# Kernel optimization log

Measured on AMD Instinct MI355X. Metric: run time of the kernel, lower is better.

## Reference

```python
import jax, jax.numpy as jnp
import numpy as np

B = 16
D = 512
LENGTHS = [2048 + 256 * i for i in range(B)]  # sum = 63488 tokens (incl. cls per bag)


def _index_maps(lengths):
    # Static (numpy) index maps for ragged <-> padded layout. Each bag's row 0 is a
    # cls token (left untouched); rows 1..L-1 are the conv body.
    lengths = [int(l) for l in np.asarray(lengths).tolist()]
    offs = np.cumsum([0] + lengths)
    lens_b = [l - 1 for l in lengths]            # body lengths after removing cls
    Lmax = max(lens_b)
    Bn = len(lengths)
    pad_src = np.zeros((Bn, Lmax), dtype=np.int32)   # flat x row gathered into [b,t]
    pad_mask = np.zeros((Bn, Lmax), dtype=np.float32)
    body_pos_list, body_b_list, body_t_list = [], [], []
    for i, L in enumerate(lens_b):
        rows = np.arange(offs[i] + 1, offs[i] + 1 + L)
        pad_src[i, :L] = rows
        pad_mask[i, :L] = 1.0
        body_pos_list.append(rows)
        body_b_list.append(np.full(L, i, dtype=np.int32))
        body_t_list.append(np.arange(L, dtype=np.int32))
    body_pos = np.concatenate(body_pos_list)   # flat positions of body tokens
    body_b = np.concatenate(body_b_list)
    body_t = np.concatenate(body_t_list)
    return pad_src, pad_mask, body_pos, body_b, body_t


def _dwconv(xp, w, b):
    # Depthwise 'same' conv1d. xp: [B, D, Lmax], w: [D, 1, k] (torch layout), b: [D].
    y = jax.lax.conv_general_dilated(
        xp, w, window_strides=(1,), padding='SAME',
        feature_group_count=xp.shape[1],
        dimension_numbers=('NCH', 'OIH', 'NCH'))
    return y + b[None, :, None]


def setup_inputs():
    key = jax.random.key(0)
    ks = jax.random.split(key, 7)
    total = sum(LENGTHS)
    x = jax.random.normal(ks[0], (total, D), jnp.float32)
    def u(k, shape, fan):  # torch Conv1d default init: U(-1/sqrt(fan_in*k), ...)
        bound = 1.0 / np.sqrt(fan)
        return jax.random.uniform(k, shape, jnp.float32, -bound, bound)
    w3, b3 = u(ks[1], (D, 1, 3), 3), u(ks[2], (D,), 3)
    w5, b5 = u(ks[3], (D, 1, 5), 5), u(ks[4], (D,), 5)
    w7, b7 = u(ks[5], (D, 1, 7), 7), u(ks[6], (D,), 7)
    lengths = np.array(LENGTHS, dtype=np.int64)
    return {'x': x, 'w3': w3, 'b3': b3, 'w5': w5, 'b5': b5,
            'w7': w7, 'b7': b7, 'lengths': lengths}


def reference(x, w3, b3, w5, b5, w7, b7, lengths):
    pad_src, pad_mask, body_pos, body_b, body_t = _index_maps(lengths)
    # Gather ragged bodies into zero-padded [B, Lmax, D]; zero padding reproduces
    # the per-segment 'same' conv boundary behavior exactly.
    xb = x[pad_src] * pad_mask[:, :, None]
    xp = jnp.transpose(xb, (0, 2, 1))  # [B, D, Lmax]
    y = xp + _dwconv(xp, w3, b3) + _dwconv(xp, w5, b5) + _dwconv(xp, w7, b7)
    body = jnp.transpose(y, (0, 2, 1))[body_b, body_t]  # flat [sum(len-1), D]
    # cls rows keep original x values; body rows replaced by residual conv sum.
    return x.at[body_pos].set(body)
```

## Files before the change

kernel.cpp:

```cpp
#include <hip/hip_runtime.h>

#define DCH 512
#define RPB 16

__global__ __launch_bounds__(128) void ppeg_dwconv_kernel(
    const float* __restrict__ x,
    const float* __restrict__ w3, const float* __restrict__ b3,
    const float* __restrict__ w5, const float* __restrict__ b5,
    const float* __restrict__ w7, const float* __restrict__ b7,
    const int* __restrict__ lengths,
    float* __restrict__ out, int n_rows, int n_bags)
{
    __shared__ int soff[32];
    if (threadIdx.x == 0) {
        int acc = 0;
        for (int i = 0; i < n_bags; ++i) { soff[i] = acc; acc += lengths[i]; }
        soff[n_bags] = acc;
    }
    __syncthreads();

    const int tid = threadIdx.x;
    const int c0  = tid * 4;

    float W[7][4], bias[4];
    #pragma unroll
    for (int q = 0; q < 4; ++q) {
        const int d = c0 + q;
        const float a0 = w7[d*7+0], a1 = w7[d*7+1], a2 = w7[d*7+2], a3 = w7[d*7+3],
                    a4 = w7[d*7+4], a5 = w7[d*7+5], a6 = w7[d*7+6];
        const float f0 = w5[d*5+0], f1 = w5[d*5+1], f2 = w5[d*5+2], f3 = w5[d*5+3], f4 = w5[d*5+4];
        const float e0 = w3[d*3+0], e1 = w3[d*3+1], e2 = w3[d*3+2];
        W[0][q] = a0;
        W[1][q] = a1 + f0;
        W[2][q] = a2 + f1 + e0;
        W[3][q] = a3 + f2 + e1 + 1.0f;
        W[4][q] = a4 + f3 + e2;
        W[5][q] = a5 + f4;
        W[6][q] = a6;
        bias[q] = b3[d] + b5[d] + b7[d];
    }

    const int r0 = blockIdx.x * RPB;
    if (r0 >= n_rows) return;

    int b = 0;
    while (b + 1 < n_bags && soff[b + 1] <= r0) ++b;

    float4 win[7];
    #pragma unroll
    for (int j = 0; j < 6; ++j) {
        const int rr = r0 - 3 + j;
        win[j] = (rr >= 0 && rr < n_rows)
                   ? *(const float4*)(x + (size_t)rr * DCH + c0)
                   : make_float4(0.f, 0.f, 0.f, 0.f);
    }

    for (int i = 0; i < RPB; ++i) {
        const int r = r0 + i;
        if (r >= n_rows) break;

        const int rr = r + 3;
        win[6] = (rr < n_rows)
                   ? *(const float4*)(x + (size_t)rr * DCH + c0)
                   : make_float4(0.f, 0.f, 0.f, 0.f);

        while (b + 1 < n_bags && soff[b + 1] <= r) ++b;
        const int t = r - soff[b] - 1;

        float4 o;
        if (t < 0) {
            o = win[3];
        } else {
            const int Lb1 = soff[b + 1] - soff[b] - 1;
            float acc0 = bias[0], acc1 = bias[1], acc2 = bias[2], acc3 = bias[3];
            #pragma unroll
            for (int dt = -3; dt <= 3; ++dt) {
                const bool valid = (t + dt >= 0) && (t + dt < Lb1);
                const float m = valid ? 1.0f : 0.0f;
                const float4 v = win[dt + 3];
                acc0 += m * W[dt + 3][0] * v.x;
                acc1 += m * W[dt + 3][1] * v.y;
                acc2 += m * W[dt + 3][2] * v.z;
                acc3 += m * W[dt + 3][3] * v.w;
            }
            o = make_float4(acc0, acc1, acc2, acc3);
        }

        *(float4*)(out + (size_t)r * DCH + c0) = o;

        #pragma unroll
        for (int j = 0; j < 6; ++j) win[j] = win[j + 1];
    }
}

extern "C" void kernel_launch(void* const* d_in, const int* in_sizes, int n_in,
                              void* d_out, int out_size, void* d_ws, size_t ws_size,
                              hipStream_t stream) {
    const float* x       = (const float*)d_in[0];
    const float* w3      = (const float*)d_in[1];
    const float* b3      = (const float*)d_in[2];
    const float* w5      = (const float*)d_in[3];
    const float* b5      = (const float*)d_in[4];
    const float* w7      = (const float*)d_in[5];
    const float* b7      = (const float*)d_in[6];
    const int*   lengths = (const int*)d_in[7];

    const int n_bags = in_sizes[7];
    const int n_rows = in_sizes[0] / DCH;
    float* out = (float*)d_out;

    const int nblocks = (n_rows + RPB - 1) / RPB;
    ppeg_dwconv_kernel<<<nblocks, 128, 0, stream>>>(
        x, w3, b3, w5, b5, w7, b7, lengths, out, n_rows, n_bags);
}
```

Before: 242.6 us.

## Process two rows per block with all window loads issued up front

```diff
diff --git a/kernel.cpp b/kernel.cpp
--- a/kernel.cpp
+++ b/kernel.cpp
@@ -1,7 +1,6 @@
 #include <hip/hip_runtime.h>
 
 #define DCH 512
-#define RPB 16
 
 __global__ __launch_bounds__(128) void ppeg_dwconv_kernel(
     const float* __restrict__ x,
@@ -22,6 +21,18 @@
     const int tid = threadIdx.x;
     const int c0  = tid * 4;
 
+    const int r0 = blockIdx.x * 2;
+    if (r0 >= n_rows) return;
+    const int r1 = r0 + 1;
+
+    float4 v[8];
+    #pragma unroll
+    for (int j = 0; j < 8; ++j) {
+        int rr = r0 - 3 + j;
+        rr = rr < 0 ? 0 : (rr >= n_rows ? n_rows - 1 : rr);
+        v[j] = *(const float4*)(x + (size_t)rr * DCH + c0);
+    }
+
     float W[7][4], bias[4];
     #pragma unroll
     for (int q = 0; q < 4; ++q) {
@@ -40,56 +51,53 @@
         bias[q] = b3[d] + b5[d] + b7[d];
     }
 
-    const int r0 = blockIdx.x * RPB;
-    if (r0 >= n_rows) return;
-
     int b = 0;
     while (b + 1 < n_bags && soff[b + 1] <= r0) ++b;
 
-    float4 win[7];
-    #pragma unroll
-    for (int j = 0; j < 6; ++j) {
-        const int rr = r0 - 3 + j;
-        win[j] = (rr >= 0 && rr < n_rows)
-                   ? *(const float4*)(x + (size_t)rr * DCH + c0)
-                   : make_float4(0.f, 0.f, 0.f, 0.f);
+    {
+        const int t   = r0 - soff[b] - 1;
+        const int Lb1 = soff[b + 1] - soff[b] - 1;
+        float4 o;
+        if (t < 0) {
+            o = v[3];
+        } else {
+            float a0 = bias[0], a1 = bias[1], a2 = bias[2], a3 = bias[3];
+            #pragma unroll
+            for (int j = 0; j < 7; ++j) {
+                const int tp = t + j - 3;
+                const float m = (tp >= 0 && tp < Lb1) ? 1.0f : 0.0f;
+                a0 += (m * W[j][0]) * v[j].x;
+                a1 += (m * W[j][1]) * v[j].y;
+                a2 += (m * W[j][2]) * v[j].z;
+                a3 += (m * W[j][3]) * v[j].w;
+            }
+            o = make_float4(a0, a1, a2, a3);
+        }
+        *(float4*)(out + (size_t)r0 * DCH + c0) = o;
     }
 
-    for (int i = 0; i < RPB; ++i) {
-        const int r = r0 + i;
-        if (r >= n_rows) break;
-
-        const int rr = r + 3;
-        win[6] = (rr < n_rows)
-                   ? *(const float4*)(x + (size_t)rr * DCH + c0)
-                   : make_float4(0.f, 0.f, 0.f, 0.f);
-
-        while (b + 1 < n_bags && soff[b + 1] <= r) ++b;
-        const int t = r - soff[b] - 1;
-
+    if (r1 < n_rows) {
+        int b1 = b;
+        while (b1 + 1 < n_bags && soff[b1 + 1] <= r1) ++b1;
+        const int t   = r1 - soff[b1] - 1;
+        const int Lb1 = soff[b1 + 1] - soff[b1] - 1;
         float4 o;
         if (t < 0) {
-            o = win[3];
+            o = v[4];
         } else {
-            const int Lb1 = soff[b + 1] - soff[b] - 1;
-            float acc0 = bias[0], acc1 = bias[1], acc2 = bias[2], acc3 = bias[3];
+            float a0 = bias[0], a1 = bias[1], a2 = bias[2], a3 = bias[3];
             #pragma unroll
-            for (int dt = -3; dt <= 3; ++dt) {
-                const bool valid = (t + dt >= 0) && (t + dt < Lb1);
-                const float m = valid ? 1.0f : 0.0f;
-                const float4 v = win[dt + 3];
-                acc0 += m * W[dt + 3][0] * v.x;
-                acc1 += m * W[dt + 3][1] * v.y;
-                acc2 += m * W[dt + 3][2] * v.z;
-                acc3 += m * W[dt + 3][3] * v.w;
+            for (int j = 0; j < 7; ++j) {
+                const int tp = t + j - 3;
+                const float m = (tp >= 0 && tp < Lb1) ? 1.0f : 0.0f;
+                a0 += (m * W[j][0]) * v[j + 1].x;
+                a1 += (m * W[j][1]) * v[j + 1].y;
+                a2 += (m * W[j][2]) * v[j + 1].z;
+                a3 += (m * W[j][3]) * v[j + 1].w;
             }
-            o = make_float4(acc0, acc1, acc2, acc3);
+            o = make_float4(a0, a1, a2, a3);
         }
-
-        *(float4*)(out + (size_t)r * DCH + c0) = o;
-
-        #pragma unroll
-        for (int j = 0; j < 6; ++j) win[j] = win[j + 1];
+        *(float4*)(out + (size_t)r1 * DCH + c0) = o;
     }
 }
 
@@ -109,7 +117,7 @@
     const int n_rows = in_sizes[0] / DCH;
     float* out = (float*)d_out;
 
-    const int nblocks = (n_rows + RPB - 1) / RPB;
+    const int nblocks = (n_rows + 1) / 2;
     ppeg_dwconv_kernel<<<nblocks, 128, 0, stream>>>(
         x, w3, b3, w5, b5, w7, b7, lengths, out, n_rows, n_bags);
 }
```

After: 309.3 us. +27.5%, slower.

## Prefetch input rows in chunks of four with larger row tiles and nontemporal stores

Applied to the files above, without the earlier changes.

```diff
diff --git a/kernel.cpp b/kernel.cpp
--- a/kernel.cpp
+++ b/kernel.cpp
@@ -1,9 +1,12 @@
 #include <hip/hip_runtime.h>
 
-#define DCH 512
-#define RPB 16
+#define DCH   512
+#define RPB   32
+#define CHUNK 4
 
-__global__ __launch_bounds__(128) void ppeg_dwconv_kernel(
+typedef float fx4 __attribute__((ext_vector_type(4)));
+
+__global__ __launch_bounds__(128, 4) void ppeg_dwconv_kernel(
     const float* __restrict__ x,
     const float* __restrict__ w3, const float* __restrict__ b3,
     const float* __restrict__ w5, const float* __restrict__ b5,
@@ -21,6 +24,10 @@
 
     const int tid = threadIdx.x;
     const int c0  = tid * 4;
+
+    const int s0 = blockIdx.x * RPB;
+    if (s0 >= n_rows) return;
+    const int s1 = (s0 + RPB < n_rows) ? s0 + RPB : n_rows;
 
     float W[7][4], bias[4];
     #pragma unroll
@@ -40,56 +47,55 @@
         bias[q] = b3[d] + b5[d] + b7[d];
     }
 
-    const int r0 = blockIdx.x * RPB;
-    if (r0 >= n_rows) return;
+    auto ldrow = [&](int rr) -> fx4 {
+        rr = rr < 0 ? 0 : (rr >= n_rows ? n_rows - 1 : rr);
+        return *(const fx4*)(x + (size_t)rr * DCH + c0);
+    };
+
+    fx4 R[10];
+    #pragma unroll
+    for (int j = 0; j < 10; ++j) R[j] = ldrow(s0 - 3 + j);
 
     int b = 0;
-    while (b + 1 < n_bags && soff[b + 1] <= r0) ++b;
+    while (b + 1 < n_bags && soff[b + 1] <= s0) ++b;
 
-    float4 win[7];
-    #pragma unroll
-    for (int j = 0; j < 6; ++j) {
-        const int rr = r0 - 3 + j;
-        win[j] = (rr >= 0 && rr < n_rows)
-                   ? *(const float4*)(x + (size_t)rr * DCH + c0)
-                   : make_float4(0.f, 0.f, 0.f, 0.f);
-    }
+    for (int rc = s0; rc < s1; rc += CHUNK) {
+        fx4 P[CHUNK];
+        #pragma unroll
+        for (int j = 0; j < CHUNK; ++j) P[j] = ldrow(rc + 7 + j);
 
-    for (int i = 0; i < RPB; ++i) {
-        const int r = r0 + i;
-        if (r >= n_rows) break;
+        #pragma unroll
+        for (int i = 0; i < CHUNK; ++i) {
+            const int r = rc + i;
+            if (r >= s1) break;
+            while (b + 1 < n_bags && soff[b + 1] <= r) ++b;
+            const int t   = r - soff[b] - 1;
+            const int Lb1 = soff[b + 1] - soff[b] - 1;
 
-        const int rr = r + 3;
-        win[6] = (rr < n_rows)
-                   ? *(const float4*)(x + (size_t)rr * DCH + c0)
-                   : make_float4(0.f, 0.f, 0.f, 0.f);
-
-        while (b + 1 < n_bags && soff[b + 1] <= r) ++b;
-        const int t = r - soff[b] - 1;
-
-        float4 o;
-        if (t < 0) {
-            o = win[3];
-        } else {
-            const int Lb1 = soff[b + 1] - soff[b] - 1;
-            float acc0 = bias[0], acc1 = bias[1], acc2 = bias[2], acc3 = bias[3];
-            #pragma unroll
-            for (int dt = -3; dt <= 3; ++dt) {
-                const bool valid = (t + dt >= 0) && (t + dt < Lb1);
-                const float m = valid ? 1.0f : 0.0f;
-                const float4 v = win[dt + 3];
-                acc0 += m * W[dt + 3][0] * v.x;
-                acc1 += m * W[dt + 3][1] * v.y;
-                acc2 += m * W[dt + 3][2] * v.z;
-                acc3 += m * W[dt + 3][3] * v.w;
+            fx4 o;
+            if (t < 0) {
+                o = R[i + 3];
+            } else {
+                float a0 = bias[0], a1 = bias[1], a2 = bias[2], a3 = bias[3];
+                #pragma unroll
+                for (int j = 0; j < 7; ++j) {
+                    const int tp = t + j - 3;
+                    const float m = (tp >= 0 && tp < Lb1) ? 1.0f : 0.0f;
+                    const fx4 v = R[i + j];
+                    a0 += (m * W[j][0]) * v.x;
+                    a1 += (m * W[j][1]) * v.y;
+                    a2 += (m * W[j][2]) * v.z;
+                    a3 += (m * W[j][3]) * v.w;
+                }
+                o = (fx4){a0, a1, a2, a3};
             }
-            o = make_float4(acc0, acc1, acc2, acc3);
+            __builtin_nontemporal_store(o, (fx4*)(out + (size_t)r * DCH + c0));
         }
 
-        *(float4*)(out + (size_t)r * DCH + c0) = o;
-
         #pragma unroll
-        for (int j = 0; j < 6; ++j) win[j] = win[j + 1];
+        for (int j = 0; j < 10 - CHUNK; ++j) R[j] = R[j + CHUNK];
+        #pragma unroll
+        for (int j = 0; j < CHUNK; ++j) R[10 - CHUNK + j] = P[j];
     }
 }
 
```

After: 249.2 us. +2.7%, slower.
